# Kernel tuning notes

Hardware: AMD Instinct MI355X
Metric: run time of the kernel (lower is better)

## Reference

```python
import jax, jax.numpy as jnp
import numpy as np

B, L, D, NLAYERS, MAX_NODES, DEG = 32, 512, 768, 3, 128, 8


def _build_graph():
    rng = np.random.default_rng(0)
    per = rng.integers(-32, 33, size=B // 2)
    sizes = np.concatenate([96 + per, 96 - per]).astype(np.int64)  # sum = 96*B = 3072, each in [64,128]
    N = int(sizes.sum())
    offs = np.concatenate([[0], np.cumsum(sizes)])
    batch = np.repeat(np.arange(B), sizes).astype(np.int64)
    pad_idx = np.zeros((B, MAX_NODES), np.int64)
    pad_mask = np.zeros((B, MAX_NODES), bool)
    src, dst = [], []
    for b in range(B):
        n = int(sizes[b])
        pad_idx[b, :n] = np.arange(offs[b], offs[b] + n)
        pad_mask[b, :n] = True
        src.append(rng.integers(offs[b], offs[b] + n, n * DEG))
        dst.append(rng.integers(offs[b], offs[b] + n, n * DEG))
    return N, batch, pad_idx, pad_mask, np.concatenate(src), np.concatenate(dst)


def setup_inputs() -> dict:
    N, batch, pad_idx, pad_mask, esrc, edst = _build_graph()
    key = jax.random.key(0)
    ks = jax.random.split(key, 8)
    s = 1.0 / np.sqrt(D)
    return {
        "x": jax.random.normal(ks[0], (N, D), jnp.float32),
        "text": jax.random.normal(ks[1], (B, L, D), jnp.float32),
        "batch_ent1_d_mask": jnp.ones((B, 1), jnp.float32),
        "batch_ent1_g_mask": jnp.ones((B, 1), jnp.float32),
        "gnn_ws": jax.random.normal(ks[2], (NLAYERS, D, D), jnp.float32) * s,
        "gnn_wn": jax.random.normal(ks[3], (NLAYERS, D, D), jnp.float32) * s,
        "gnn_b": jnp.zeros((NLAYERS, D), jnp.float32),
        "atom_w": jax.random.normal(ks[4], (D, D), jnp.float32) * s,
        "atom_b": jnp.zeros((D,), jnp.float32),
        "rand_emb": jax.random.normal(ks[5], (1, D), jnp.float32),
        "batch": jnp.asarray(batch),
        "pad_idx": jnp.asarray(pad_idx),
        "pad_mask": jnp.asarray(pad_mask),
        "edge_src": jnp.asarray(esrc),
        "edge_dst": jnp.asarray(edst),
    }


def reference(x, text, batch_ent1_d_mask, batch_ent1_g_mask, gnn_ws, gnn_wn, gnn_b,
              atom_w, atom_b, rand_emb, batch, pad_idx, pad_mask, edge_src, edge_dst):
    N = x.shape[0]
    E = edge_src.shape[0]
    maskf = pad_mask.astype(x.dtype)            # [B, M]
    n_per = maskf.sum(axis=1)                   # [B] num real nodes per graph
    # edge-neighbor mean counts (constants w.r.t. x)
    cnt = jax.ops.segment_sum(jnp.ones((E,), x.dtype), edge_dst, num_segments=N)
    inv_cnt = 1.0 / jnp.maximum(cnt, 1.0)
    cms = []
    for i in range(NLAYERS):
        # MoleGraphConv stand-in: mean neighbor aggregation + self transform
        msg = jax.ops.segment_sum(x[edge_src], edge_dst, num_segments=N) * inv_cnt[:, None]
        x = jax.nn.relu(x @ gnn_ws[i] + msg @ gnn_wn[i] + gnn_b[i])
        # ragged gather into padded [B, M, D]
        xp = x[pad_idx] * maskf[..., None]
        # graph -> text cross attention (softmax over text tokens; no mask needed)
        g2t = jax.nn.softmax(jnp.einsum('bmd,bld->bml', xp, text), axis=-1)
        g2t_out = jnp.einsum('bml,bld->bmd', g2t, text)            # [B, M, D]
        # text -> graph cross attention (mask padded nodes)
        t2g_logits = jnp.einsum('bld,bmd->blm', text, xp)
        t2g_logits = jnp.where(pad_mask[:, None, :], t2g_logits, jnp.float32(-1e9))
        t2g = jax.nn.softmax(t2g_logits, axis=-1)
        t2g_out = jnp.einsum('blm,bmd->bld', t2g, xp)              # [B, L, D]
        # mean over concatenated rows [n_i + L] per graph (pool_type=2)
        pooled = ((g2t_out * maskf[..., None]).sum(axis=1) + t2g_out.sum(axis=1)) \
                 / (n_per + jnp.float32(L))[:, None]
        cms.append(pooled)
    out_cms = jnp.mean(jnp.stack(cms, axis=1), axis=1)              # mean over layers
    out_t = text[:, 0, :]
    # scatter-mean of final node features per graph
    gsum = jax.ops.segment_sum(x, batch, num_segments=B)
    gcnt = jax.ops.segment_sum(jnp.ones((N,), x.dtype), batch, num_segments=B)
    xg = gsum / jnp.maximum(gcnt, 1.0)[:, None]
    # dropout is a no-op in eval mode
    out_g = jnp.tanh(xg @ atom_w + atom_b)
    z = rand_emb[0]
    dg = batch_ent1_d_mask * batch_ent1_g_mask
    return jnp.concatenate([
        out_t * batch_ent1_d_mask + (1 - batch_ent1_d_mask) * z,
        out_g * batch_ent1_g_mask + (1 - batch_ent1_g_mask) * z,
        out_cms * dg + (1 - dg) * z,
    ], axis=-1)
```

## Files before the change

### kernel.cpp

```cpp
#include <hip/hip_runtime.h>

#define D 768
#define B 32
#define L 512
#define M 128
#define NNODES 3072
#define NEDGES 24576

using bf16x8 = __attribute__((ext_vector_type(8))) short;
using f32x4  = __attribute__((ext_vector_type(4))) float;

__device__ __forceinline__ float bf2f(unsigned short u) {
  union { unsigned int i; float f; } v; v.i = ((unsigned int)u) << 16; return v.f;
}
__device__ __forceinline__ unsigned short f2bf(float f) {
  union { float f; unsigned int i; } v; v.f = f;
  unsigned int x = v.i;
  return (unsigned short)((x + 0x7FFFu + ((x >> 16) & 1u)) >> 16);
}
__device__ __forceinline__ float ldf(const void* p, size_t i, int f32) {
  return f32 ? ((const float*)p)[i] : bf2f(((const unsigned short*)p)[i]);
}
__device__ __forceinline__ int ldi(const void* p, size_t i, int w64) {
  return w64 ? (int)((const long long*)p)[i] : ((const int*)p)[i];
}
__device__ __forceinline__ f32x4 mfma16(bf16x8 a, bf16x8 b, f32x4 c) {
  return __builtin_amdgcn_mfma_f32_16x16x32_bf16(a, b, c, 0, 0, 0);
}

__device__ __forceinline__ float pk_read(const unsigned short* P, int p, int l, int d) {
  return bf2f(P[(((size_t)(p * 24 + (d >> 5))) << 9) + ((((d & 31) >> 3) << 4) + l) * 8 + (d & 7)]);
}

__device__ __forceinline__ void fma8(float* acc, float w, uint4 v) {
  unsigned xs[4] = {v.x, v.y, v.z, v.w};
#pragma unroll
  for (int j = 0; j < 4; ++j) {
    acc[2 * j]     += w * bf2f((unsigned short)(xs[j] & 0xFFFFu));
    acc[2 * j + 1] += w * bf2f((unsigned short)(xs[j] >> 16));
  }
}

__device__ __forceinline__ void acc12(float* a, const uint2* u) {
#pragma unroll
  for (int j = 0; j < 3; ++j) {
    a[j * 4 + 0] += bf2f((unsigned short)(u[j].x & 0xFFFFu));
    a[j * 4 + 1] += bf2f((unsigned short)(u[j].x >> 16));
    a[j * 4 + 2] += bf2f((unsigned short)(u[j].y & 0xFFFFu));
    a[j * 4 + 3] += bf2f((unsigned short)(u[j].y >> 16));
  }
}


__device__ void d_pack_in(const void* src, unsigned short* rows, unsigned short* dst,
                          int p, int tid, int f) {
  unsigned short* pb = dst + (size_t)p * 12288;
#pragma unroll
  for (int j = 0; j < 6; ++j) {
    int odx = j * 256 + tid;
    int kk = odx >> 6, lanep = odx & 63;
    int q = lanep >> 4, r16 = lanep & 15;
    int row = p * 16 + r16, col0 = kk * 32 + q * 8;
    size_t sbase = (size_t)row * 768 + col0;
    union { unsigned short v[8]; uint4 qv; } u;
    if (f) {
      const float* sp = (const float*)src + sbase;
      float4 v0 = *(const float4*)sp;
      float4 v1 = *(const float4*)(sp + 4);
      u.v[0] = f2bf(v0.x); u.v[1] = f2bf(v0.y); u.v[2] = f2bf(v0.z); u.v[3] = f2bf(v0.w);
      u.v[4] = f2bf(v1.x); u.v[5] = f2bf(v1.y); u.v[6] = f2bf(v1.z); u.v[7] = f2bf(v1.w);
    } else {
      u.qv = *(const uint4*)((const unsigned short*)src + sbase);
    }
    if (rows) *(uint4*)&rows[sbase] = u.qv;
    *(uint4*)&pb[(size_t)odx * 8] = u.qv;
  }
}

__device__ void d_pack(const unsigned short* src, unsigned short* dst,
                       int p, int tid) {
  unsigned short* pb = dst + (size_t)p * 12288;
#pragma unroll
  for (int j = 0; j < 6; ++j) {
    int odx = j * 256 + tid;
    int kk = odx >> 6, lanep = odx & 63;
    int q = lanep >> 4, r16 = lanep & 15;
    size_t sbase = (size_t)(p * 16 + r16) * 768 + kk * 32 + q * 8;
    uint4 qv = *(const uint4*)(src + sbase);
    *(uint4*)&pb[(size_t)odx * 8] = qv;
  }
}

__device__ void d_wpack(const void* Ws, const void* Wn, const void* Aw, int f,
                        unsigned short* WsPk, unsigned short* WnPk, unsigned short* AwPk,
                        int r0, int tid) {
  int z = r0 / 288, rem = r0 % 288;
  int nblk = rem % 12, kk = rem / 12;
  const void* src; unsigned short* dst; size_t zoff;
  if (z < 3)      { src = Ws; zoff = (size_t)z * D * D;       dst = WsPk + zoff; }
  else if (z < 6) { src = Wn; zoff = (size_t)(z - 3) * D * D; dst = WnPk + zoff; }
  else            { src = Aw; zoff = 0;                       dst = AwPk; }
  int pl = tid >> 6, lane = tid & 63;
  int pG = nblk * 4 + pl;
  int k0 = kk * 32 + ((lane >> 4) << 3);
  int n  = nblk * 64 + pl * 16 + (lane & 15);
  union { unsigned short v[8]; uint4 q; } u;
  if (f) {
    const float* sp = (const float*)src + zoff + (size_t)k0 * D + n;
#pragma unroll
    for (int e = 0; e < 8; ++e) u.v[e] = f2bf(sp[(size_t)e * D]);
  } else {
    const unsigned short* sp = (const unsigned short*)src + zoff + (size_t)k0 * D + n;
#pragma unroll
    for (int e = 0; e < 8; ++e) u.v[e] = sp[(size_t)e * D];
  }
  *(uint4*)&dst[(((size_t)(pG * 24 + kk)) << 9) + lane * 8] = u.q;
}

__device__ void d_count(const void* edst, const void* batch, int w,
                        int* cnt, int* gcnt, int i) {
  if (i < NEDGES) atomicAdd(&cnt[ldi(edst, i, w)], 1);
  if (i < NNODES) {
    int b = ldi(batch, i, w);
    int lane = i & 63;
    int prev = __shfl_up(b, 1);
    bool first = (lane == 0) || (prev != b);
    unsigned long long bm = __ballot(first ? 1 : 0);
    if (first) {
      unsigned long long higher = (lane < 63) ? (bm >> (lane + 1)) : 0ULL;
      int next = higher ? (lane + __ffsll((long long)higher)) : 64;
      atomicAdd(&gcnt[b], next - lane);
    }
  }
}

__device__ void d_msg(const unsigned short* x, const int* cnt, const int* rowstart,
                      const int* csr, unsigned short* Mpk, int p, int tid) {
  int w = tid >> 6, lane = tid & 63;
  unsigned short* pb = Mpk + (size_t)p * 12288;
#pragma unroll
  for (int i = 0; i < 4; i += 2) {
    int rA = w * 4 + i, rB = rA + 1;
    int nA = p * 16 + rA, nB = p * 16 + rB;
    int degA = cnt[nA], baseA = rowstart[nA];
    int degB = cnt[nB], baseB = rowstart[nB];
    float aA[12], aB[12];
#pragma unroll
    for (int j = 0; j < 12; ++j) { aA[j] = 0.f; aB[j] = 0.f; }
    int dmax = degA > degB ? degA : degB;
    for (int e = 0; e < dmax; ++e) {
      uint2 uA[3], uB[3];
      if (e < degA) {
        const uint2* xr = (const uint2*)(x + (size_t)csr[baseA + e] * D);
        uA[0] = xr[lane]; uA[1] = xr[lane + 64]; uA[2] = xr[lane + 128];
      }
      if (e < degB) {
        const uint2* xr = (const uint2*)(x + (size_t)csr[baseB + e] * D);
        uB[0] = xr[lane]; uB[1] = xr[lane + 64]; uB[2] = xr[lane + 128];
      }
      if (e < degA) acc12(aA, uA);
      if (e < degB) acc12(aB, uB);
    }
    float invA = 1.0f / (float)(degA > 1 ? degA : 1);
    float invB = 1.0f / (float)(degB > 1 ? degB : 1);
#pragma unroll
    for (int j = 0; j < 3; ++j) {
      int d0 = (lane + j * 64) * 4;
      int kk = d0 >> 5, q = (d0 >> 3) & 3, e0 = d0 & 7;
      uint2 wA, wB;
      wA.x = (unsigned int)f2bf(aA[j * 4 + 0] * invA)
           | ((unsigned int)f2bf(aA[j * 4 + 1] * invA) << 16);
      wA.y = (unsigned int)f2bf(aA[j * 4 + 2] * invA)
           | ((unsigned int)f2bf(aA[j * 4 + 3] * invA) << 16);
      wB.x = (unsigned int)f2bf(aB[j * 4 + 0] * invB)
           | ((unsigned int)f2bf(aB[j * 4 + 1] * invB) << 16);
      wB.y = (unsigned int)f2bf(aB[j * 4 + 2] * invB)
           | ((unsigned int)f2bf(aB[j * 4 + 3] * invB) << 16);
      *(uint2*)&pb[kk * 512 + (q * 16 + rA) * 8 + e0] = wA;
      *(uint2*)&pb[kk * 512 + (q * 16 + rB) * 8 + e0] = wB;
    }
  }
}

__device__ void d_gemm(const unsigned short* Xpk, const unsigned short* Mpk,
                       const unsigned short* WsPk, const unsigned short* WnPk,
                       const void* bias, size_t bias_off, int f,
                       unsigned short* Y, int bx, int by, int tid) {
  int wave = tid >> 6, lane = tid & 63;
  int q = lane >> 4, t = lane & 15;
  int wm = wave >> 1, wn = wave & 1;
  const int PAN = 24 << 9;
  f32x4 acc[2][2];
#pragma unroll
  for (int mi = 0; mi < 2; ++mi)
#pragma unroll
    for (int ni = 0; ni < 2; ++ni)
      acc[mi][ni] = (f32x4){0.f, 0.f, 0.f, 0.f};
  size_t aoff = (((size_t)((bx * 4 + wm * 2) * 24)) << 9) + lane * 8;
  size_t boff = (((size_t)((by * 4 + wn * 2) * 24)) << 9) + lane * 8;
  {
    const unsigned short* A = Xpk + aoff;
    const unsigned short* Bp = WsPk + boff;
#pragma unroll 4
    for (int kk = 0; kk < 24; ++kk) {
      bf16x8 a0 = *(const bf16x8*)(A + kk * 512);
      bf16x8 a1 = *(const bf16x8*)(A + kk * 512 + PAN);
      bf16x8 b0 = *(const bf16x8*)(Bp + kk * 512);
      bf16x8 b1 = *(const bf16x8*)(Bp + kk * 512 + PAN);
      acc[0][0] = mfma16(a0, b0, acc[0][0]);
      acc[0][1] = mfma16(a0, b1, acc[0][1]);
      acc[1][0] = mfma16(a1, b0, acc[1][0]);
      acc[1][1] = mfma16(a1, b1, acc[1][1]);
    }
  }
  {
    const unsigned short* A = Mpk + aoff;
    const unsigned short* Bp = WnPk + boff;
#pragma unroll 4
    for (int kk = 0; kk < 24; ++kk) {
      bf16x8 a0 = *(const bf16x8*)(A + kk * 512);
      bf16x8 a1 = *(const bf16x8*)(A + kk * 512 + PAN);
      bf16x8 b0 = *(const bf16x8*)(Bp + kk * 512);
      bf16x8 b1 = *(const bf16x8*)(Bp + kk * 512 + PAN);
      acc[0][0] = mfma16(a0, b0, acc[0][0]);
      acc[0][1] = mfma16(a0, b1, acc[0][1]);
      acc[1][0] = mfma16(a1, b0, acc[1][0]);
      acc[1][1] = mfma16(a1, b1, acc[1][1]);
    }
  }
#pragma unroll
  for (int ni = 0; ni < 2; ++ni) {
    int col = by * 64 + wn * 32 + ni * 16 + t;
    float bv = ldf(bias, bias_off + col, f);
#pragma unroll
    for (int mi = 0; mi < 2; ++mi) {
#pragma unroll
      for (int r = 0; r < 4; ++r) {
        int row = bx * 64 + wm * 32 + mi * 16 + q * 4 + r;
        float v = acc[mi][ni][r] + bv;
        Y[(size_t)row * D + col] = f2bf(v > 0.f ? v : 0.f);
      }
    }
  }
}

__device__ void d_xp(const unsigned short* Xn, const void* pidx, int w64,
                     const int* gcnt, unsigned short* xp, unsigned short* XpPk,
                     float* xgacc, int p, int tid, char* smem) {
  unsigned short* rows = (unsigned short*)smem;
  int r = tid >> 4, c16 = tid & 15;
  int bm = p * 16 + r;
  int b = bm >> 7, m = bm & 127;
  int nb = gcnt[b];
  uint4* dl = (uint4*)&rows[r * 776];
  uint4 v[6];
  if (m < nb) {
    const uint4* srcr = (const uint4*)(Xn + (size_t)ldi(pidx, bm, w64) * D);
#pragma unroll
    for (int j = 0; j < 6; ++j) v[j] = srcr[c16 + j * 16];
  } else {
    uint4 z = {0u, 0u, 0u, 0u};
#pragma unroll
    for (int j = 0; j < 6; ++j) v[j] = z;
  }
#pragma unroll
  for (int j = 0; j < 6; ++j) dl[c16 + j * 16] = v[j];
  __syncthreads();
#pragma unroll
  for (int j = 0; j < 6; ++j) {
    int idx = j * 256 + tid;
    int rr = idx / 96, cc = idx % 96;
    uint4 vv = *(const uint4*)&rows[rr * 776 + cc * 8];
    *(uint4*)&xp[(size_t)(p * 16 + rr) * D + cc * 8] = vv;
  }
  unsigned short* pb = XpPk + (size_t)p * 12288;
#pragma unroll
  for (int j = 0; j < 6; ++j) {
    int odx = j * 256 + tid;
    int kk = odx >> 6, lanep = odx & 63;
    int rr = lanep & 15, cg = lanep >> 4;
    int cc = kk * 4 + cg;
    uint4 vv = *(const uint4*)&rows[rr * 776 + cc * 8];
    *(uint4*)&pb[odx * 8] = vv;
  }
  if (xgacc) {
    int bb = p >> 3;
#pragma unroll
    for (int j = 0; j < 3; ++j) {
      int d = j * 256 + tid;
      float s = 0.f;
#pragma unroll
      for (int rr = 0; rr < 16; ++rr) s += bf2f(rows[rr * 776 + d]);
      atomicAdd(&xgacc[(size_t)bb * D + d], s);
    }
  }
}

__device__ void d_scores(const unsigned short* XpPk, const unsigned short* Tpk,
                         float* S, int bx, int by, int bz, int tid) {
  int wave = tid >> 6, lane = tid & 63;
  int q = lane >> 4, t = lane & 15;
  int wm = wave >> 1, wn = wave & 1;
  const int PAN = 24 << 9;
  f32x4 acc[2][2];
#pragma unroll
  for (int mi = 0; mi < 2; ++mi)
#pragma unroll
    for (int ni = 0; ni < 2; ++ni)
      acc[mi][ni] = (f32x4){0.f, 0.f, 0.f, 0.f};
  size_t aoff = (((size_t)((bz * 8 + bx * 4 + wm * 2) * 24)) << 9) + lane * 8;
  size_t boff = (((size_t)((bz * 32 + by * 4 + wn * 2) * 24)) << 9) + lane * 8;
  const unsigned short* A = XpPk + aoff;
  const unsigned short* Bp = Tpk + boff;
#pragma unroll 4
  for (int kk = 0; kk < 24; ++kk) {
    bf16x8 a0 = *(const bf16x8*)(A + kk * 512);
    bf16x8 a1 = *(const bf16x8*)(A + kk * 512 + PAN);
    bf16x8 b0 = *(const bf16x8*)(Bp + kk * 512);
    bf16x8 b1 = *(const bf16x8*)(Bp + kk * 512 + PAN);
    acc[0][0] = mfma16(a0, b0, acc[0][0]);
    acc[0][1] = mfma16(a0, b1, acc[0][1]);
    acc[1][0] = mfma16(a1, b0, acc[1][0]);
    acc[1][1] = mfma16(a1, b1, acc[1][1]);
  }
  float* Sb = S + (size_t)bz * M * L;
#pragma unroll
  for (int ni = 0; ni < 2; ++ni) {
    int col = by * 64 + wn * 32 + ni * 16 + t;
#pragma unroll
    for (int mi = 0; mi < 2; ++mi) {
#pragma unroll
      for (int r = 0; r < 4; ++r) {
        int row = bx * 64 + wm * 32 + mi * 16 + q * 4 + r;
        Sb[(size_t)row * L + col] = acc[mi][ni][r];
      }
    }
  }
}

__device__ void d_stats(const float* S, const int* gcnt, float* rmax, float* rsum,
                        float* cmaxv, float* csumv, int bid, int tid, char* smem) {
  if (bid < B * M) {
    float* red = (float*)smem;
    int lane = tid & 63, wv = tid >> 6;
    const float* r = S + (size_t)bid * L;
    float s0 = r[tid], s1 = r[tid + 256];
    float m = fmaxf(s0, s1);
#pragma unroll
    for (int o = 32; o > 0; o >>= 1) m = fmaxf(m, __shfl_down(m, o));
    if (lane == 0) red[wv] = m;
    __syncthreads();
    float bm = fmaxf(fmaxf(red[0], red[1]), fmaxf(red[2], red[3]));
    __syncthreads();
    float e = __expf(s0 - bm) + __expf(s1 - bm);
#pragma unroll
    for (int o = 32; o > 0; o >>= 1) e += __shfl_down(e, o);
    if (lane == 0) red[wv] = e;
    __syncthreads();
    if (tid == 0) { rmax[bid] = bm; rsum[bid] = red[0] + red[1] + red[2] + red[3]; }
  } else {
    float (*pm)[64] = (float(*)[64])smem;
    float (*ps)[64] = (float(*)[64])(smem + 1024);
    int cid = bid - B * M;
    int b = cid >> 3, ly = cid & 7;
    int w = tid >> 6, lane = tid & 63;
    int l = ly * 64 + lane;
    int nb = gcnt[b];
    const float* Sb = S + (size_t)b * M * L;
    int m0 = w * 32, m1 = min(m0 + 32, nb);
    float cm = -1e30f, cs = 0.f;
    for (int m = m0; m < m1; ++m) {
      float s = Sb[(size_t)m * L + l];
      if (s > cm) { cs = cs * __expf(cm - s) + 1.f; cm = s; }
      else cs += __expf(s - cm);
    }
    pm[w][lane] = cm; ps[w][lane] = cs;
    __syncthreads();
    if (w == 0) {
      float CM = -1e30f;
#pragma unroll
      for (int j = 0; j < 4; ++j) CM = fmaxf(CM, pm[j][lane]);
      float CS = 0.f;
#pragma unroll
      for (int j = 0; j < 4; ++j) CS += ps[j][lane] * __expf(pm[j][lane] - CM);
      cmaxv[b * L + l] = CM; csumv[b * L + l] = CS;
    }
  }
}

__device__ void d_cross(const float* S, const float* rmax, const float* rsum,
                        const float* cmaxv, const float* csumv, const int* gcnt,
                        float* wv, float* t2gcol, int bid, int tid, char* smem) {
  if (bid < 256) {
    float* rm = (float*)smem;
    float* ri = (float*)(smem + 512);
    float (*pw)[64] = (float(*)[64])(smem + 1024);
    int b = bid >> 3, ly = bid & 7;
    int w = tid >> 6, lane = tid & 63;
    if (tid < M) { rm[tid] = rmax[b * M + tid]; ri[tid] = 1.f / rsum[b * M + tid]; }
    __syncthreads();
    int l = ly * 64 + lane;
    int nb = gcnt[b];
    const float* Sb = S + (size_t)b * M * L;
    int m0 = w * 32, m1 = min(m0 + 32, nb);
    float wp = 0.f;
    for (int m = m0; m < m1; ++m)
      wp += __expf(Sb[(size_t)m * L + l] - rm[m]) * ri[m];
    pw[w][lane] = wp;
    __syncthreads();
    if (w == 0)
      wv[b * L + l] = pw[0][lane] + pw[1][lane] + pw[2][lane] + pw[3][lane];
  } else {
    float* red = (float*)smem;
    int bm = bid - 256;
    int b = bm >> 7, m = bm & 127;
    int lane = tid & 63, w = tid >> 6;
    int nb = gcnt[b];
    float acc = 0.f;
    if (m < nb) {
      const float* r = S + (size_t)bm * L;
      const float* cm = cmaxv + b * L;
      const float* cs = csumv + b * L;
      acc = __expf(r[tid] - cm[tid]) / cs[tid]
          + __expf(r[tid + 256] - cm[tid + 256]) / cs[tid + 256];
    }
#pragma unroll
    for (int o = 32; o > 0; o >>= 1) acc += __shfl_down(acc, o);
    if (lane == 0) red[w] = acc;
    __syncthreads();
    if (tid == 0) t2gcol[bm] = red[0] + red[1] + red[2] + red[3];
  }
}

__device__ void d_pooled(const float* wv, const float* t2gcol, const unsigned short* Tpk,
                         const unsigned short* xp, const int* gcnt, float* pooled,
                         int bid, int tid, char* smem) {
  float* lred = (float*)smem;
  float* wbuf = (float*)(smem + 3072);
  int b = bid / 10, seg = bid - b * 10;
  int chunk = tid % 96, half = tid / 96;
  int d = chunk * 8;
  float acc[8];
#pragma unroll
  for (int j = 0; j < 8; ++j) acc[j] = 0.f;
  if (tid < 64) {
    wbuf[tid] = (seg < 8) ? wv[b * L + seg * 64 + tid]
                          : t2gcol[b * M + (seg - 8) * 64 + tid];
  }
  __syncthreads();
  if (half < 2) {
    if (seg < 8) {
      int pbase = b * 32 + seg * 4;
      size_t cbase = ((size_t)(d >> 5)) << 9;
      int coff = ((d & 31) >> 3) << 4;
      for (int i = 0; i < 32; ++i) {
        int l = half * 32 + i;
        const unsigned short* src =
            Tpk + (((size_t)((pbase + (l >> 4)) * 24)) << 9) + cbase +
            (size_t)(coff + (l & 15)) * 8;
        fma8(acc, wbuf[l], *(const uint4*)src);
      }
    } else {
      const unsigned short* Xb = xp + (size_t)b * M * D + d;
      int m0 = (seg - 8) * 64;
      for (int i = 0; i < 32; ++i) {
        int mm = half * 32 + i;
        fma8(acc, wbuf[mm], *(const uint4*)&Xb[(size_t)(m0 + mm) * D]);
      }
    }
  }
  if (half == 1) {
#pragma unroll
    for (int j = 0; j < 8; ++j) lred[chunk * 8 + j] = acc[j];
  }
  __syncthreads();
  if (half == 0) {
    float inv = 1.f / ((float)gcnt[b] + 512.f);
#pragma unroll
    for (int j = 0; j < 8; ++j)
      atomicAdd(&pooled[(size_t)b * D + d + j], (acc[j] + lred[chunk * 8 + j]) * inv);
  }
}

__device__ void d_atom(const float* xgacc, const int* gcnt, const unsigned short* AwPk,
                       float* gpre, int bid, int tid) {
  int w = tid >> 6, lane = tid & 63;
  int q = lane >> 4, t = lane & 15;
  int nbase = bid * 64 + w * 16;
  int pb = nbase >> 4;
  int n0 = gcnt[t], n1 = gcnt[16 + t];
  float inv0 = 1.f / (float)(n0 > 1 ? n0 : 1);
  float inv1 = 1.f / (float)(n1 > 1 ? n1 : 1);
  f32x4 acc[2];
  acc[0] = (f32x4){0.f, 0.f, 0.f, 0.f};
  acc[1] = (f32x4){0.f, 0.f, 0.f, 0.f};
  for (int kk = 0; kk < 24; ++kk) {
    const float* s0 = xgacc + (size_t)t * D + kk * 32 + q * 8;
    const float* s1 = xgacc + (size_t)(16 + t) * D + kk * 32 + q * 8;
    union { unsigned short v[8]; bf16x8 f; } a0, a1;
#pragma unroll
    for (int j = 0; j < 8; ++j) { a0.v[j] = f2bf(s0[j] * inv0); a1.v[j] = f2bf(s1[j] * inv1); }
    bf16x8 bv = *(const bf16x8*)(AwPk + (((size_t)(pb * 24 + kk)) << 9) + (lane << 3));
    acc[0] = mfma16(a0.f, bv, acc[0]);
    acc[1] = mfma16(a1.f, bv, acc[1]);
  }
#pragma unroll
  for (int mi = 0; mi < 2; ++mi)
#pragma unroll
    for (int r = 0; r < 4; ++r) {
      int row = mi * 16 + q * 4 + r;
      gpre[(size_t)row * D + nbase + t] = acc[mi][r];
    }
}


__global__ void k_init(int* cnt, int* cursor, int* gcnt, float* pooled, float* xgacc,
                       const unsigned short* __restrict__ t,
                       const unsigned int* __restrict__ e, int* __restrict__ flags) {
  int i = blockIdx.x * 256 + threadIdx.x;
  if (i < NNODES) { cnt[i] = 0; cursor[i] = 0; }
  if (i < B) gcnt[i] = 0;
  if (i < B * D) { pooled[i] = 0.f; xgacc[i] = 0.f; }
  if (blockIdx.x == 0) {
    __shared__ int r0[256];
    __shared__ unsigned r1[256];
    int tid = threadIdx.x;
    int bad = 0;
    for (int j = tid; j < 8192; j += 256) {
      unsigned short u = t[2 * j];
      unsigned ex = (u >> 7) & 0xFF;
      if (ex >= 0xC0) bad = 1;
    }
    unsigned o = 0;
    for (int j = tid; j < NEDGES / 2; j += 256) o |= e[2 * j + 1];
    r0[tid] = bad; r1[tid] = o;
    __syncthreads();
    for (int s = 128; s > 0; s >>= 1) {
      if (tid < s) { r0[tid] |= r0[tid + s]; r1[tid] |= r1[tid + s]; }
      __syncthreads();
    }
    if (tid == 0) { flags[0] = r0[0]; flags[1] = (r1[0] == 0) ? 1 : 0; }
  }
}

__global__ __launch_bounds__(256) void k_setup2(
    const void* x_in, unsigned short* x0, unsigned short* PkA,
    const void* text, unsigned short* Tpk,
    const void* Ws, const void* Wn, const void* Aw,
    unsigned short* WsPk, unsigned short* WnPk, unsigned short* AwPk,
    const void* edst, const void* batch, int* cnt, int* gcnt,
    const int* __restrict__ flags) {
  int bid = blockIdx.x, tid = threadIdx.x;
  if (bid < 1216) {
    int f = flags[0];
    if (bid < NNODES / 16) d_pack_in(x_in, x0, PkA, bid, tid, f);
    else d_pack_in(text, nullptr, Tpk, bid - NNODES / 16, tid, f);
  } else if (bid < 3232) {
    d_wpack(Ws, Wn, Aw, flags[0], WsPk, WnPk, AwPk, bid - 1216, tid);
  } else {
    d_count(edst, batch, flags[1], cnt, gcnt, (bid - 3232) * 256 + tid);
  }
}

__global__ void k_scan(const int* __restrict__ cnt, int* __restrict__ rowstart) {
  __shared__ int a[NNODES], b[NNODES];
  int tid = threadIdx.x;
  for (int i = tid; i < NNODES; i += 1024) a[i] = cnt[i];
  __syncthreads();
  int* s = a; int* d = b;
  for (int off = 1; off < NNODES; off <<= 1) {
    for (int i = tid; i < NNODES; i += 1024)
      d[i] = s[i] + (i >= off ? s[i - off] : 0);
    __syncthreads();
    int* t = s; s = d; d = t;
  }
  for (int i = tid; i < NNODES; i += 1024) rowstart[i + 1] = s[i];
  if (tid == 0) rowstart[0] = 0;
}

__global__ void k_scatter(const void* __restrict__ esrc, const void* __restrict__ edst,
                          const int* __restrict__ flags, const int* __restrict__ rowstart,
                          int* __restrict__ cursor, int* __restrict__ csr) {
  int w = flags[1];
  int i = blockIdx.x * 256 + threadIdx.x;
  if (i < NEDGES) {
    int dd = ldi(edst, i, w);
    int pos = atomicAdd(&cursor[dd], 1);
    csr[rowstart[dd] + pos] = ldi(esrc, i, w);
  }
}

__global__ __launch_bounds__(256) void k_msgp(
    const unsigned short* x, const int* cnt, const int* rowstart, const int* csr,
    unsigned short* Mpk) {
  d_msg(x, cnt, rowstart, csr, Mpk, blockIdx.x, threadIdx.x);
}

__device__ __forceinline__ void gemm_map(int g, int& bx, int& by) {
  int gs = (g % 8) * 72 + g / 8;
  bx = gs / 12; by = gs % 12;
}
__device__ __forceinline__ void sc_map(int g, int& bx, int& by, int& bz) {
  int gs = (g % 8) * 64 + g / 8;
  bx = gs & 1; by = (gs >> 1) & 7; bz = gs >> 4;
}

__global__ __launch_bounds__(256) void k_gemm(
    const unsigned short* Apk, const unsigned short* Mpk,
    const unsigned short* WsPk, const unsigned short* WnPk,
    const void* bias, unsigned long bias_off, const int* flags, unsigned short* Y) {
  int bx, by; gemm_map(blockIdx.x, bx, by);
  d_gemm(Apk, Mpk, WsPk, WnPk, bias, bias_off, flags[0], Y, bx, by, threadIdx.x);
}

__global__ __launch_bounds__(256) void k_postg(
    const unsigned short* Y, unsigned short* Npk, int packN,
    const void* pidx, const int* flags, const int* gcnt,
    unsigned short* xp, unsigned short* XpPk, float* xgacc) {
  extern __shared__ char smem[];
  int bid = blockIdx.x, tid = threadIdx.x;
  if (bid < packN) d_pack(Y, Npk, bid, tid);
  else d_xp(Y, pidx, flags[1], gcnt, xp, XpPk, xgacc, bid - packN, tid, smem);
}

__global__ __launch_bounds__(256) void k_scmsg(
    const unsigned short* XpPk, const unsigned short* Tpk, float* S,
    int msgN, const unsigned short* x, const int* cnt, const int* rowstart,
    const int* csr, unsigned short* Mpk) {
  int bid = blockIdx.x, tid = threadIdx.x;
  if (bid < 512) {
    int bx, by, bz; sc_map(bid, bx, by, bz);
    d_scores(XpPk, Tpk, S, bx, by, bz, tid);
  } else d_msg(x, cnt, rowstart, csr, Mpk, bid - 512, tid);
}

__global__ __launch_bounds__(256) void k_stgemm(
    const float* S, const int* gcnt, float* rmax, float* rsum, float* cmaxv, float* csumv,
    int gemmN, const unsigned short* Apk, const unsigned short* Mpk,
    const unsigned short* WsPk, const unsigned short* WnPk,
    const void* bias, unsigned long bias_off, const int* flags, unsigned short* Y) {
  extern __shared__ char smem[];
  int bid = blockIdx.x, tid = threadIdx.x;
  if (bid < 4352) d_stats(S, gcnt, rmax, rsum, cmaxv, csumv, bid, tid, smem);
  else {
    int bx, by; gemm_map(bid - 4352, bx, by);
    d_gemm(Apk, Mpk, WsPk, WnPk, bias, bias_off, flags[0], Y, bx, by, tid);
  }
}

__global__ __launch_bounds__(256) void k_crpostg(
    const float* S, const float* rmax, const float* rsum, const float* cmaxv,
    const float* csumv, const int* gcnt, float* wv, float* t2gcol,
    int packN, int xpN, const unsigned short* Y, unsigned short* Npk,
    const void* pidx, const int* flags, unsigned short* xp, unsigned short* XpPk,
    float* xgacc) {
  extern __shared__ char smem[];
  int bid = blockIdx.x, tid = threadIdx.x;
  if (bid < 4352) d_cross(S, rmax, rsum, cmaxv, csumv, gcnt, wv, t2gcol, bid, tid, smem);
  else {
    int r = bid - 4352;
    if (r < packN) d_pack(Y, Npk, r, tid);
    else d_xp(Y, pidx, flags[1], gcnt, xp, XpPk, xgacc, r - packN, tid, smem);
  }
}

__global__ __launch_bounds__(256) void k_plscmsg(
    const float* wv, const float* t2gcol, const unsigned short* Tpk,
    const unsigned short* xpL, const int* gcnt, float* pooled,
    int scN, const unsigned short* XpPk, float* S,
    int msgN, const unsigned short* x, const int* cnt, const int* rowstart,
    const int* csr, unsigned short* Mpk,
    int atomN, const float* xgacc, const unsigned short* AwPk, float* gpre) {
  extern __shared__ char smem[];
  int bid = blockIdx.x, tid = threadIdx.x;
  if (bid < 320) { d_pooled(wv, t2gcol, Tpk, xpL, gcnt, pooled, bid, tid, smem); return; }
  int r = bid - 320;
  if (r < scN) {
    int bx, by, bz; sc_map(r, bx, by, bz);
    d_scores(XpPk, Tpk, S, bx, by, bz, tid); return;
  }
  r -= scN;
  if (r < msgN) { d_msg(x, cnt, rowstart, csr, Mpk, r, tid); return; }
  d_atom(xgacc, gcnt, AwPk, gpre, r - msgN, tid);
}

__global__ __launch_bounds__(256) void k_final(
    const unsigned short* __restrict__ Tpk, const float* __restrict__ gpre,
    const float* __restrict__ pooled, const void* __restrict__ ab,
    const void* __restrict__ dmask, const void* __restrict__ gmask,
    const void* __restrict__ remb, const int* __restrict__ flags,
    void* __restrict__ out) {
  int f = flags[0];
  int b = blockIdx.x, tid = threadIdx.x;
  float dm = ldf(dmask, b, f);
  float gm = ldf(gmask, b, f);
  float dg = dm * gm;
  size_t base = (size_t)b * 2304;
#pragma unroll
  for (int j = 0; j < 3; ++j) {
    int d = tid + j * 256;
    float z = ldf(remb, d, f);
    float tv = pk_read(Tpk, b * 32, 0, d);
    float o0 = tv * dm + (1.f - dm) * z;
    float gv = tanhf(gpre[(size_t)b * D + d] + ldf(ab, d, f));
    float o1 = gv * gm + (1.f - gm) * z;
    float p = pooled[(size_t)b * D + d] * (1.f / 3.f);
    float o2 = p * dg + (1.f - dg) * z;
    if (f) {
      float* of = (float*)out;
      of[base + d] = o0; of[base + 768 + d] = o1; of[base + 1536 + d] = o2;
    } else {
      unsigned short* ob = (unsigned short*)out;
      ob[base + d] = f2bf(o0); ob[base + 768 + d] = f2bf(o1); ob[base + 1536 + d] = f2bf(o2);
    }
  }
}

extern "C" void kernel_launch(void* const* d_in, const int* in_sizes, int n_in,
                              void* d_out, int out_size, void* d_ws, size_t ws_size,
                              hipStream_t stream) {
  const void* x_in  = d_in[0];
  const void* text  = d_in[1];
  const void* dmask = d_in[2];
  const void* gmask = d_in[3];
  const void* gws   = d_in[4];
  const void* gwn   = d_in[5];
  const void* gb    = d_in[6];
  const void* aw    = d_in[7];
  const void* ab    = d_in[8];
  const void* remb  = d_in[9];
  const void* batch = d_in[10];
  const void* pidx  = d_in[11];
  const void* esrc  = d_in[13];
  const void* edst  = d_in[14];

  char* wsp = (char*)d_ws;
  size_t off = 0;
  auto carve = [&](size_t bytes) -> void* {
    void* p = wsp + off;
    off += (bytes + 255) & ~(size_t)255;
    return p;
  };
  int* flags = (int*)carve(2 * 4);
  unsigned short* x0    = (unsigned short*)carve((size_t)NNODES * D * 2);
  unsigned short* xA    = (unsigned short*)carve((size_t)NNODES * D * 2);
  unsigned short* xB    = (unsigned short*)carve((size_t)NNODES * D * 2);
  unsigned short* PkA   = (unsigned short*)carve((size_t)NNODES * D * 2);
  unsigned short* PkB   = (unsigned short*)carve((size_t)NNODES * D * 2);
  unsigned short* Mpk   = (unsigned short*)carve((size_t)NNODES * D * 2);
  unsigned short* Tpk   = (unsigned short*)carve((size_t)B * L * D * 2);
  unsigned short* WsPk  = (unsigned short*)carve((size_t)3 * D * D * 2);
  unsigned short* WnPk  = (unsigned short*)carve((size_t)3 * D * D * 2);
  unsigned short* AwPk  = (unsigned short*)carve((size_t)D * D * 2);
  unsigned short* xpA   = (unsigned short*)carve((size_t)B * M * D * 2);
  unsigned short* xpB   = (unsigned short*)carve((size_t)B * M * D * 2);
  unsigned short* XpPkA = (unsigned short*)carve((size_t)B * M * D * 2);
  unsigned short* XpPkB = (unsigned short*)carve((size_t)B * M * D * 2);
  float* xgacc   = (float*)carve((size_t)B * D * 4);
  float* gpre    = (float*)carve((size_t)B * D * 4);
  float* S       = (float*)carve((size_t)B * M * L * 4);
  float* rmax    = (float*)carve((size_t)B * M * 4);
  float* rsum    = (float*)carve((size_t)B * M * 4);
  float* wv      = (float*)carve((size_t)B * L * 4);
  float* cmaxv   = (float*)carve((size_t)B * L * 4);
  float* csumv   = (float*)carve((size_t)B * L * 4);
  float* t2gcol  = (float*)carve((size_t)B * M * 4);
  float* pooled  = (float*)carve((size_t)B * D * 4);
  int* cnt      = (int*)carve((size_t)NNODES * 4);
  int* rowstart = (int*)carve((size_t)(NNODES + 1) * 4);
  int* cursor   = (int*)carve((size_t)NNODES * 4);
  int* gcnt     = (int*)carve((size_t)B * 4);
  int* csr      = (int*)carve((size_t)NEDGES * 4);

  const size_t DD = (size_t)D * D;

  k_init<<<96, 256, 0, stream>>>(cnt, cursor, gcnt, pooled, xgacc,
                                 (const unsigned short*)text, (const unsigned int*)edst, flags);
  k_setup2<<<3328, 256, 0, stream>>>(x_in, x0, PkA, text, Tpk, gws, gwn, aw,
                                     WsPk, WnPk, AwPk, edst, batch, cnt, gcnt, flags);
  k_scan<<<1, 1024, 0, stream>>>(cnt, rowstart);
  k_scatter<<<96, 256, 0, stream>>>(esrc, edst, flags, rowstart, cursor, csr);

  k_msgp<<<192, 256, 0, stream>>>(x0, cnt, rowstart, csr, Mpk);
  k_gemm<<<576, 256, 0, stream>>>(PkA, Mpk, WsPk, WnPk, gb, 0, flags, xA);
  k_postg<<<448, 256, 24832, stream>>>(xA, PkB, 192, pidx, flags, gcnt, xpA, XpPkA, nullptr);
  k_scmsg<<<704, 256, 0, stream>>>(XpPkA, Tpk, S, 192, xA, cnt, rowstart, csr, Mpk);
  k_stgemm<<<4928, 256, 2048, stream>>>(S, gcnt, rmax, rsum, cmaxv, csumv,
                                        576, PkB, Mpk, WsPk + DD, WnPk + DD, gb, D, flags, xB);
  k_crpostg<<<4800, 256, 24832, stream>>>(S, rmax, rsum, cmaxv, csumv, gcnt, wv, t2gcol,
                                          192, 256, xB, PkA, pidx, flags, xpB, XpPkB, nullptr);
  k_plscmsg<<<1024, 256, 4096, stream>>>(wv, t2gcol, Tpk, xpA, gcnt, pooled,
                                         512, XpPkB, S, 192, xB, cnt, rowstart, csr, Mpk,
                                         0, nullptr, nullptr, nullptr);
  k_stgemm<<<4928, 256, 2048, stream>>>(S, gcnt, rmax, rsum, cmaxv, csumv,
                                        576, PkA, Mpk, WsPk + 2 * DD, WnPk + 2 * DD,
                                        gb, 2 * D, flags, xA);
  k_crpostg<<<4608, 256, 24832, stream>>>(S, rmax, rsum, cmaxv, csumv, gcnt, wv, t2gcol,
                                          0, 256, xA, nullptr, pidx, flags, xpA, XpPkA, xgacc);
  k_plscmsg<<<832, 256, 4096, stream>>>(wv, t2gcol, Tpk, xpB, gcnt, pooled,
                                        512, XpPkA, S, 0, nullptr, nullptr, nullptr,
                                        nullptr, nullptr, 0, nullptr, nullptr, nullptr);
  k_stgemm<<<4352, 256, 2048, stream>>>(S, gcnt, rmax, rsum, cmaxv, csumv,
                                        0, nullptr, nullptr, nullptr, nullptr,
                                        nullptr, 0, flags, nullptr);
  k_crpostg<<<4352, 256, 2048, stream>>>(S, rmax, rsum, cmaxv, csumv, gcnt, wv, t2gcol,
                                         0, 0, nullptr, nullptr, pidx, flags,
                                         nullptr, nullptr, nullptr);
  k_plscmsg<<<332, 256, 4096, stream>>>(wv, t2gcol, Tpk, xpA, gcnt, pooled,
                                        0, nullptr, nullptr, 0, nullptr, nullptr, nullptr,
                                        nullptr, nullptr, 12, xgacc, AwPk, gpre);
  k_final<<<32, 256, 0, stream>>>(Tpk, gpre, pooled, ab, dmask, gmask, remb, flags, d_out);
}
```

Measured before the change: 421.2 us.

## Fuse packed-layout output into GEMM epilogue and reorder fused-kernel block roles

```diff
diff --git a/kernel.cpp b/kernel.cpp
--- a/kernel.cpp
+++ b/kernel.cpp
@@ -74,20 +74,6 @@
     }
     if (rows) *(uint4*)&rows[sbase] = u.qv;
     *(uint4*)&pb[(size_t)odx * 8] = u.qv;
-  }
-}
-
-__device__ void d_pack(const unsigned short* src, unsigned short* dst,
-                       int p, int tid) {
-  unsigned short* pb = dst + (size_t)p * 12288;
-#pragma unroll
-  for (int j = 0; j < 6; ++j) {
-    int odx = j * 256 + tid;
-    int kk = odx >> 6, lanep = odx & 63;
-    int q = lanep >> 4, r16 = lanep & 15;
-    size_t sbase = (size_t)(p * 16 + r16) * 768 + kk * 32 + q * 8;
-    uint4 qv = *(const uint4*)(src + sbase);
-    *(uint4*)&pb[(size_t)odx * 8] = qv;
   }
 }
 
@@ -138,46 +124,43 @@
                       const int* csr, unsigned short* Mpk, int p, int tid) {
   int w = tid >> 6, lane = tid & 63;
   unsigned short* pb = Mpk + (size_t)p * 12288;
-#pragma unroll
-  for (int i = 0; i < 4; i += 2) {
-    int rA = w * 4 + i, rB = rA + 1;
-    int nA = p * 16 + rA, nB = p * 16 + rB;
-    int degA = cnt[nA], baseA = rowstart[nA];
-    int degB = cnt[nB], baseB = rowstart[nB];
-    float aA[12], aB[12];
-#pragma unroll
-    for (int j = 0; j < 12; ++j) { aA[j] = 0.f; aB[j] = 0.f; }
-    int dmax = degA > degB ? degA : degB;
-    for (int e = 0; e < dmax; ++e) {
-      uint2 uA[3], uB[3];
-      if (e < degA) {
-        const uint2* xr = (const uint2*)(x + (size_t)csr[baseA + e] * D);
-        uA[0] = xr[lane]; uA[1] = xr[lane + 64]; uA[2] = xr[lane + 128];
+  int deg[4], base[4];
+  float a[4][12];
+#pragma unroll
+  for (int r4 = 0; r4 < 4; ++r4) {
+    int n = p * 16 + w * 4 + r4;
+    deg[r4] = cnt[n]; base[r4] = rowstart[n];
+#pragma unroll
+    for (int j = 0; j < 12; ++j) a[r4][j] = 0.f;
+  }
+  int dmax = max(max(deg[0], deg[1]), max(deg[2], deg[3]));
+  for (int e = 0; e < dmax; ++e) {
+    uint2 u[4][3];
+#pragma unroll
+    for (int r4 = 0; r4 < 4; ++r4) {
+      if (e < deg[r4]) {
+        const uint2* xr = (const uint2*)(x + (size_t)csr[base[r4] + e] * D);
+        u[r4][0] = xr[lane]; u[r4][1] = xr[lane + 64]; u[r4][2] = xr[lane + 128];
       }
-      if (e < degB) {
-        const uint2* xr = (const uint2*)(x + (size_t)csr[baseB + e] * D);
-        uB[0] = xr[lane]; uB[1] = xr[lane + 64]; uB[2] = xr[lane + 128];
-      }
-      if (e < degA) acc12(aA, uA);
-      if (e < degB) acc12(aB, uB);
-    }
-    float invA = 1.0f / (float)(degA > 1 ? degA : 1);
-    float invB = 1.0f / (float)(degB > 1 ? degB : 1);
+    }
+#pragma unroll
+    for (int r4 = 0; r4 < 4; ++r4)
+      if (e < deg[r4]) acc12(a[r4], u[r4]);
+  }
+#pragma unroll
+  for (int r4 = 0; r4 < 4; ++r4) {
+    int rA = w * 4 + r4;
+    float inv = 1.0f / (float)(deg[r4] > 1 ? deg[r4] : 1);
 #pragma unroll
     for (int j = 0; j < 3; ++j) {
       int d0 = (lane + j * 64) * 4;
       int kk = d0 >> 5, q = (d0 >> 3) & 3, e0 = d0 & 7;
-      uint2 wA, wB;
-      wA.x = (unsigned int)f2bf(aA[j * 4 + 0] * invA)
-           | ((unsigned int)f2bf(aA[j * 4 + 1] * invA) << 16);
-      wA.y = (unsigned int)f2bf(aA[j * 4 + 2] * invA)
-           | ((unsigned int)f2bf(aA[j * 4 + 3] * invA) << 16);
-      wB.x = (unsigned int)f2bf(aB[j * 4 + 0] * invB)
-           | ((unsigned int)f2bf(aB[j * 4 + 1] * invB) << 16);
-      wB.y = (unsigned int)f2bf(aB[j * 4 + 2] * invB)
-           | ((unsigned int)f2bf(aB[j * 4 + 3] * invB) << 16);
-      *(uint2*)&pb[kk * 512 + (q * 16 + rA) * 8 + e0] = wA;
-      *(uint2*)&pb[kk * 512 + (q * 16 + rB) * 8 + e0] = wB;
+      uint2 wv;
+      wv.x = (unsigned int)f2bf(a[r4][j * 4 + 0] * inv)
+           | ((unsigned int)f2bf(a[r4][j * 4 + 1] * inv) << 16);
+      wv.y = (unsigned int)f2bf(a[r4][j * 4 + 2] * inv)
+           | ((unsigned int)f2bf(a[r4][j * 4 + 3] * inv) << 16);
+      *(uint2*)&pb[kk * 512 + (q * 16 + rA) * 8 + e0] = wv;
     }
   }
 }
@@ -185,7 +168,7 @@
 __device__ void d_gemm(const unsigned short* Xpk, const unsigned short* Mpk,
                        const unsigned short* WsPk, const unsigned short* WnPk,
                        const void* bias, size_t bias_off, int f,
-                       unsigned short* Y, int bx, int by, int tid) {
+                       unsigned short* Y, unsigned short* Ypk, int bx, int by, int tid) {
   int wave = tid >> 6, lane = tid & 63;
   int q = lane >> 4, t = lane & 15;
   int wm = wave >> 1, wn = wave & 1;
@@ -232,13 +215,23 @@
   for (int ni = 0; ni < 2; ++ni) {
     int col = by * 64 + wn * 32 + ni * 16 + t;
     float bv = ldf(bias, bias_off + col, f);
+    int kkc = col >> 5, cq = (col >> 3) & 3, ec = col & 7;
 #pragma unroll
     for (int mi = 0; mi < 2; ++mi) {
+      unsigned short us[4];
 #pragma unroll
       for (int r = 0; r < 4; ++r) {
         int row = bx * 64 + wm * 32 + mi * 16 + q * 4 + r;
         float v = acc[mi][ni][r] + bv;
-        Y[(size_t)row * D + col] = f2bf(v > 0.f ? v : 0.f);
+        us[r] = f2bf(v > 0.f ? v : 0.f);
+        Y[(size_t)row * D + col] = us[r];
+      }
+      if (Ypk) {
+        int pOut = bx * 4 + wm * 2 + mi;
+        unsigned short* ob = Ypk + (size_t)pOut * 12288 + kkc * 512 + ec;
+#pragma unroll
+        for (int r = 0; r < 4; ++r)
+          ob[(cq * 16 + q * 4 + r) * 8] = us[r];
       }
     }
   }
@@ -608,19 +601,17 @@
 __global__ __launch_bounds__(256) void k_gemm(
     const unsigned short* Apk, const unsigned short* Mpk,
     const unsigned short* WsPk, const unsigned short* WnPk,
-    const void* bias, unsigned long bias_off, const int* flags, unsigned short* Y) {
+    const void* bias, unsigned long bias_off, const int* flags,
+    unsigned short* Y, unsigned short* Ypk) {
   int bx, by; gemm_map(blockIdx.x, bx, by);
-  d_gemm(Apk, Mpk, WsPk, WnPk, bias, bias_off, flags[0], Y, bx, by, threadIdx.x);
+  d_gemm(Apk, Mpk, WsPk, WnPk, bias, bias_off, flags[0], Y, Ypk, bx, by, threadIdx.x);
 }
 
 __global__ __launch_bounds__(256) void k_postg(
-    const unsigned short* Y, unsigned short* Npk, int packN,
-    const void* pidx, const int* flags, const int* gcnt,
+    const unsigned short* Y, const void* pidx, const int* flags, const int* gcnt,
     unsigned short* xp, unsigned short* XpPk, float* xgacc) {
   extern __shared__ char smem[];
-  int bid = blockIdx.x, tid = threadIdx.x;
-  if (bid < packN) d_pack(Y, Npk, bid, tid);
-  else d_xp(Y, pidx, flags[1], gcnt, xp, XpPk, xgacc, bid - packN, tid, smem);
+  d_xp(Y, pidx, flags[1], gcnt, xp, XpPk, xgacc, blockIdx.x, threadIdx.x, smem);
 }
 
 __global__ __launch_bounds__(256) void k_scmsg(
@@ -628,60 +619,56 @@
     int msgN, const unsigned short* x, const int* cnt, const int* rowstart,
     const int* csr, unsigned short* Mpk) {
   int bid = blockIdx.x, tid = threadIdx.x;
-  if (bid < 512) {
-    int bx, by, bz; sc_map(bid, bx, by, bz);
+  if (bid < msgN) d_msg(x, cnt, rowstart, csr, Mpk, bid, tid);
+  else {
+    int bx, by, bz; sc_map(bid - msgN, bx, by, bz);
     d_scores(XpPk, Tpk, S, bx, by, bz, tid);
-  } else d_msg(x, cnt, rowstart, csr, Mpk, bid - 512, tid);
+  }
 }
 
 __global__ __launch_bounds__(256) void k_stgemm(
     const float* S, const int* gcnt, float* rmax, float* rsum, float* cmaxv, float* csumv,
     int gemmN, const unsigned short* Apk, const unsigned short* Mpk,
     const unsigned short* WsPk, const unsigned short* WnPk,
-    const void* bias, unsigned long bias_off, const int* flags, unsigned short* Y) {
+    const void* bias, unsigned long bias_off, const int* flags,
+    unsigned short* Y, unsigned short* Ypk) {
   extern __shared__ char smem[];
   int bid = blockIdx.x, tid = threadIdx.x;
-  if (bid < 4352) d_stats(S, gcnt, rmax, rsum, cmaxv, csumv, bid, tid, smem);
-  else {
-    int bx, by; gemm_map(bid - 4352, bx, by);
-    d_gemm(Apk, Mpk, WsPk, WnPk, bias, bias_off, flags[0], Y, bx, by, tid);
-  }
+  if (bid < gemmN) {
+    int bx, by; gemm_map(bid, bx, by);
+    d_gemm(Apk, Mpk, WsPk, WnPk, bias, bias_off, flags[0], Y, Ypk, bx, by, tid);
+  } else d_stats(S, gcnt, rmax, rsum, cmaxv, csumv, bid - gemmN, tid, smem);
 }
 
 __global__ __launch_bounds__(256) void k_crpostg(
     const float* S, const float* rmax, const float* rsum, const float* cmaxv,
     const float* csumv, const int* gcnt, float* wv, float* t2gcol,
-    int packN, int xpN, const unsigned short* Y, unsigned short* Npk,
-    const void* pidx, const int* flags, unsigned short* xp, unsigned short* XpPk,
-    float* xgacc) {
+    int xpN, const unsigned short* Y, const void* pidx, const int* flags,
+    unsigned short* xp, unsigned short* XpPk, float* xgacc) {
   extern __shared__ char smem[];
   int bid = blockIdx.x, tid = threadIdx.x;
-  if (bid < 4352) d_cross(S, rmax, rsum, cmaxv, csumv, gcnt, wv, t2gcol, bid, tid, smem);
-  else {
-    int r = bid - 4352;
-    if (r < packN) d_pack(Y, Npk, r, tid);
-    else d_xp(Y, pidx, flags[1], gcnt, xp, XpPk, xgacc, r - packN, tid, smem);
-  }
+  if (bid < xpN) d_xp(Y, pidx, flags[1], gcnt, xp, XpPk, xgacc, bid, tid, smem);
+  else d_cross(S, rmax, rsum, cmaxv, csumv, gcnt, wv, t2gcol, bid - xpN, tid, smem);
 }
 
 __global__ __launch_bounds__(256) void k_plscmsg(
     const float* wv, const float* t2gcol, const unsigned short* Tpk,
     const unsigned short* xpL, const int* gcnt, float* pooled,
-    int scN, const unsigned short* XpPk, float* S,
     int msgN, const unsigned short* x, const int* cnt, const int* rowstart,
     const int* csr, unsigned short* Mpk,
+    int scN, const unsigned short* XpPk, float* S,
     int atomN, const float* xgacc, const unsigned short* AwPk, float* gpre) {
   extern __shared__ char smem[];
   int bid = blockIdx.x, tid = threadIdx.x;
-  if (bid < 320) { d_pooled(wv, t2gcol, Tpk, xpL, gcnt, pooled, bid, tid, smem); return; }
-  int r = bid - 320;
+  if (bid < msgN) { d_msg(x, cnt, rowstart, csr, Mpk, bid, tid); return; }
+  int r = bid - msgN;
   if (r < scN) {
     int bx, by, bz; sc_map(r, bx, by, bz);
     d_scores(XpPk, Tpk, S, bx, by, bz, tid); return;
   }
   r -= scN;
-  if (r < msgN) { d_msg(x, cnt, rowstart, csr, Mpk, r, tid); return; }
-  d_atom(xgacc, gcnt, AwPk, gpre, r - msgN, tid);
+  if (r < 320) { d_pooled(wv, t2gcol, Tpk, xpL, gcnt, pooled, r, tid, smem); return; }
+  d_atom(xgacc, gcnt, AwPk, gpre, r - 320, tid);
 }
 
 __global__ __launch_bounds__(256) void k_final(
@@ -782,32 +769,35 @@
   k_scatter<<<96, 256, 0, stream>>>(esrc, edst, flags, rowstart, cursor, csr);
 
   k_msgp<<<192, 256, 0, stream>>>(x0, cnt, rowstart, csr, Mpk);
-  k_gemm<<<576, 256, 0, stream>>>(PkA, Mpk, WsPk, WnPk, gb, 0, flags, xA);
-  k_postg<<<448, 256, 24832, stream>>>(xA, PkB, 192, pidx, flags, gcnt, xpA, XpPkA, nullptr);
+  k_gemm<<<576, 256, 0, stream>>>(PkA, Mpk, WsPk, WnPk, gb, 0, flags, xA, PkB);
+  k_postg<<<256, 256, 24832, stream>>>(xA, pidx, flags, gcnt, xpA, XpPkA, nullptr);
   k_scmsg<<<704, 256, 0, stream>>>(XpPkA, Tpk, S, 192, xA, cnt, rowstart, csr, Mpk);
   k_stgemm<<<4928, 256, 2048, stream>>>(S, gcnt, rmax, rsum, cmaxv, csumv,
-                                        576, PkB, Mpk, WsPk + DD, WnPk + DD, gb, D, flags, xB);
-  k_crpostg<<<4800, 256, 24832, stream>>>(S, rmax, rsum, cmaxv, csumv, gcnt, wv, t2gcol,
-                                          192, 256, xB, PkA, pidx, flags, xpB, XpPkB, nullptr);
+                                        576, PkB, Mpk, WsPk + DD, WnPk + DD, gb, D, flags,
+                                        xB, PkA);
+  k_crpostg<<<4608, 256, 24832, stream>>>(S, rmax, rsum, cmaxv, csumv, gcnt, wv, t2gcol,
+                                          256, xB, pidx, flags, xpB, XpPkB, nullptr);
   k_plscmsg<<<1024, 256, 4096, stream>>>(wv, t2gcol, Tpk, xpA, gcnt, pooled,
-                                         512, XpPkB, S, 192, xB, cnt, rowstart, csr, Mpk,
+                                         192, xB, cnt, rowstart, csr, Mpk,
+                                         512, XpPkB, S,
                                          0, nullptr, nullptr, nullptr);
   k_stgemm<<<4928, 256, 2048, stream>>>(S, gcnt, rmax, rsum, cmaxv, csumv,
                                         576, PkA, Mpk, WsPk + 2 * DD, WnPk + 2 * DD,
-                                        gb, 2 * D, flags, xA);
+                                        gb, 2 * D, flags, xA, nullptr);
   k_crpostg<<<4608, 256, 24832, stream>>>(S, rmax, rsum, cmaxv, csumv, gcnt, wv, t2gcol,
-                                          0, 256, xA, nullptr, pidx, flags, xpA, XpPkA, xgacc);
+                                          256, xA, pidx, flags, xpA, XpPkA, xgacc);
   k_plscmsg<<<832, 256, 4096, stream>>>(wv, t2gcol, Tpk, xpB, gcnt, pooled,
-                                        512, XpPkA, S, 0, nullptr, nullptr, nullptr,
-                                        nullptr, nullptr, 0, nullptr, nullptr, nullptr);
+                                        0, nullptr, nullptr, nullptr, nullptr, nullptr,
+                                        512, XpPkA, S,
+                                        0, nullptr, nullptr, nullptr);
   k_stgemm<<<4352, 256, 2048, stream>>>(S, gcnt, rmax, rsum, cmaxv, csumv,
                                         0, nullptr, nullptr, nullptr, nullptr,
-                                        nullptr, 0, flags, nullptr);
+                                        nullptr, 0, flags, nullptr, nullptr);
   k_crpostg<<<4352, 256, 2048, stream>>>(S, rmax, rsum, cmaxv, csumv, gcnt, wv, t2gcol,
-                                         0, 0, nullptr, nullptr, pidx, flags,
-                                         nullptr, nullptr, nullptr);
+                                         0, nullptr, pidx, flags, nullptr, nullptr, nullptr);
   k_plscmsg<<<332, 256, 4096, stream>>>(wv, t2gcol, Tpk, xpA, gcnt, pooled,
-                                        0, nullptr, nullptr, 0, nullptr, nullptr, nullptr,
-                                        nullptr, nullptr, 12, xgacc, AwPk, gpre);
+                                        0, nullptr, nullptr, nullptr, nullptr, nullptr,
+                                        0, nullptr, nullptr,
+                                        12, xgacc, AwPk, gpre);
   k_final<<<32, 256, 0, stream>>>(Tpk, gpre, pooled, ab, dmask, gmask, remb, flags, d_out);
 }
```

Result: faster. 412.0 us (median of 2 runs) (-2.2%).
